# Performance work log

Measured on AMD Instinct MI355X. Metric: run time of the kernel, lower is better.

## Reference

```python
import jax, jax.numpy as jnp
import numpy as np

N_NODES = 100000
N_EDGES = 1000000
NHID = 128
N_CLASSES = 5000


def setup_inputs() -> dict:
    key = jax.random.key(0)
    ks = jax.random.split(key, 8)
    feature = jax.random.normal(ks[0], (N_NODES, NHID), dtype=jnp.float32)
    # Linear weights stored as [in, out] so forward is x @ W + b
    W1 = jax.random.normal(ks[1], (2 * NHID, NHID), dtype=jnp.float32) * (1.0 / np.sqrt(2 * NHID))
    b1 = jnp.zeros((NHID,), dtype=jnp.float32)
    alpha = jnp.full((NHID,), 0.25, dtype=jnp.float32)  # PReLU per-channel init
    W2 = jax.random.normal(ks[2], (NHID, 2), dtype=jnp.float32) * (1.0 / np.sqrt(NHID))
    b2 = jnp.zeros((2,), dtype=jnp.float32)
    row = jax.random.randint(ks[3], (N_EDGES,), 0, N_NODES, dtype=jnp.int64)
    col = jax.random.randint(ks[4], (N_EDGES,), 0, N_NODES, dtype=jnp.int64)
    label = jax.random.randint(ks[5], (N_NODES,), 0, N_CLASSES, dtype=jnp.int64)
    return {"feature": feature, "W1": W1, "b1": b1, "alpha": alpha,
            "W2": W2, "b2": b2, "row": row, "col": col, "label": label}


def reference(feature, W1, b1, alpha, W2, b2, row, col, label):
    # per-edge label: 1 if endpoints share a cluster label
    y = (label[row] == label[col]).astype(jnp.int32)  # [E]
    # edge gather + concat: [E, 2*nhid]
    x = jnp.concatenate([feature[row], feature[col]], axis=1)
    h = x @ W1 + b1                                   # [E, nhid]
    h = jnp.where(h >= 0, h, alpha * h)               # PReLU, per-channel alpha
    logits = h @ W2 + b2                              # [E, 2]
    logp = jax.nn.log_softmax(logits, axis=-1)
    # mean cross-entropy over edges
    loss = -jnp.mean(jnp.take_along_axis(logp, y[:, None], axis=1))
    return loss
```

## Files before the change

kernel.cpp:

```cpp
#include <hip/hip_runtime.h>
#include <hip/hip_bf16.h>

typedef __bf16 bf16_t;
typedef bf16_t bf16x8 __attribute__((ext_vector_type(8)));
typedef float floatx4 __attribute__((ext_vector_type(4)));
typedef float floatx2 __attribute__((ext_vector_type(2)));

#define N_NODES 100000
#define N_EDGES 1000000
#define NHID 128
#define PQ_COLS 256

__global__ __launch_bounds__(256) void k_prep(const float* __restrict__ W1,
                                              const float* __restrict__ b1,
                                              const float* __restrict__ alpha,
                                              const float* __restrict__ W2,
                                              const float* __restrict__ b2,
                                              bf16_t* __restrict__ WT,
                                              float* __restrict__ wabsg,
                                              float* __restrict__ u1g,
                                              float* __restrict__ u2g,
                                              float* __restrict__ constg) {
    __shared__ float w1L[128];
    int i = blockIdx.x * 256 + threadIdx.x;
    if (i < 32768) {
        int n = i >> 7;
        int k = i & 127;
        float v = (n < 128) ? W1[k * 128 + n] : W1[(k + 128) * 128 + (n - 128)];
        WT[i] = (bf16_t)v;
    }
    if (blockIdx.x == 128) {
        int t = threadIdx.x;
        if (t < 128) {
            float wd = W2[2 * t + 1] - W2[2 * t];
            float al = alpha[t];
            w1L[t] = wd * (1.f + al) * 0.5f;
            wabsg[t] = wd * (1.f - al) * 0.5f;
        }
        __syncthreads();
        if (t < 128) {
            float a1 = 0.f, a2 = 0.f;
            for (int j = 0; j < 128; ++j) {
                a1 = fmaf(W1[t * 128 + j], w1L[j], a1);
                a2 = fmaf(W1[(t + 128) * 128 + j], w1L[j], a2);
            }
            u1g[t] = a1;
            u2g[t] = a2;
        }
        if (t == 0) {
            float c = 0.f;
            for (int j = 0; j < 128; ++j) c = fmaf(w1L[j], b1[j], c);
            *constg = c + (b2[1] - b2[0]);
        }
    }
}

__global__ __launch_bounds__(256) void k_gemm_pq(const float* __restrict__ F,
                                                 const bf16_t* __restrict__ WT,
                                                 const float* __restrict__ b1,
                                                 const float* __restrict__ u1g,
                                                 const float* __restrict__ u2g,
                                                 const int* __restrict__ label,
                                                 unsigned char* __restrict__ PQ8,
                                                 float4* __restrict__ aux_g) {
    __shared__ bf16x8 As8[1024];
    __shared__ float sp1[4][64];
    __shared__ float sp2[4][64];
    const int t = threadIdx.x;
    const int m0 = blockIdx.x * 64;

#pragma unroll
    for (int j = 0; j < 8; ++j) {
        int chunk = j * 256 + t;
        int r = chunk >> 5;
        int c4 = chunk & 31;
        int gr = m0 + r;
        float4 u = {0.f, 0.f, 0.f, 0.f};
        if (gr < N_NODES) u = ((const float4*)F)[(size_t)gr * 32 + c4];
        int s    = c4 >> 3;
        int quad = (c4 >> 1) & 3;
        int half = c4 & 1;
        bf16_t* dst = (bf16_t*)&As8[(((r >> 4) * 4 + s) * 4 + quad) * 16 + (r & 15)] + half * 4;
        dst[0] = (bf16_t)u.x; dst[1] = (bf16_t)u.y; dst[2] = (bf16_t)u.z; dst[3] = (bf16_t)u.w;
    }
    __syncthreads();

    const int wave = t >> 6, lane = t & 63;
    const int l15 = lane & 15, quad = lane >> 4;
    const int n0 = wave * 64;

    float bias_v[4];
#pragma unroll
    for (int nt = 0; nt < 4; ++nt) {
        int n = n0 + nt * 16 + l15;
        bias_v[nt] = (n < 128) ? b1[n] : 0.f;
    }

    floatx4 acc[4][4] = {};
#pragma unroll
    for (int s = 0; s < 4; ++s) {
        bf16x8 a[4], b[4];
#pragma unroll
        for (int mt = 0; mt < 4; ++mt)
            a[mt] = As8[(mt * 4 + s) * 64 + lane];
#pragma unroll
        for (int nt = 0; nt < 4; ++nt)
            b[nt] = *(const bf16x8*)(WT + (size_t)(n0 + nt * 16 + l15) * NHID + s * 32 + quad * 8);
#pragma unroll
        for (int mt = 0; mt < 4; ++mt)
#pragma unroll
            for (int nt = 0; nt < 4; ++nt)
                acc[mt][nt] = __builtin_amdgcn_mfma_f32_16x16x32_bf16(a[mt], b[nt], acc[mt][nt], 0, 0, 0);
    }

    {
        int rr = t & 63, part = t >> 6;
        int mt_ = rr >> 4, r15 = rr & 15;
        float a1 = 0.f, a2 = 0.f;
#pragma unroll
        for (int qd = 0; qd < 4; ++qd) {
            bf16x8 av = As8[((mt_ * 4 + part) * 4 + qd) * 16 + r15];
#pragma unroll
            for (int idx = 0; idx < 8; ++idx) {
                float fv = (float)av[idx];
                int kk = part * 32 + qd * 8 + idx;
                a1 = fmaf(fv, u1g[kk], a1);
                a2 = fmaf(fv, u2g[kk], a2);
            }
        }
        sp1[part][rr] = a1;
        sp2[part][rr] = a2;
    }
    __syncthreads();
    if (t < 64) {
        int grow = m0 + t;
        if (grow < N_NODES) {
            float s1 = (sp1[0][t] + sp1[1][t]) + (sp1[2][t] + sp1[3][t]);
            float s2 = (sp2[0][t] + sp2[1][t]) + (sp2[2][t] + sp2[3][t]);
            float4 av = {s1, s2, __int_as_float(label[grow]), 0.f};
            aux_g[grow] = av;
        }
    }

    bf16_t* Tb = (bf16_t*)As8;
#pragma unroll
    for (int h = 0; h < 2; ++h) {
        __syncthreads();
#pragma unroll
        for (int mi = 0; mi < 2; ++mi) {
            int mt = h * 2 + mi;
#pragma unroll
            for (int r = 0; r < 4; ++r) {
                int rl = mi * 16 + quad * 4 + r;
                int sw = ((rl >> 2) & 3) << 4;
#pragma unroll
                for (int nt = 0; nt < 4; ++nt) {
                    int colx = n0 + nt * 16 + l15;
                    Tb[rl * 256 + (colx ^ sw)] = (bf16_t)(acc[mt][nt][r] + bias_v[nt]);
                }
            }
        }
        __syncthreads();
#pragma unroll
        for (int j = 0; j < 4; ++j) {
            int chunk = j * 256 + t;
            int rl  = chunk >> 5;
            int c16 = chunk & 31;
            int grow = m0 + h * 32 + rl;
            if (grow < N_NODES) {
                bf16x8 v = ((bf16x8*)Tb)[rl * 32 + (c16 ^ ((rl >> 2) & 3) * 2)];
                unsigned int lo = 0, hi = 0;
                lo = __builtin_amdgcn_cvt_pk_fp8_f32((float)v[0], (float)v[1], lo, false);
                lo = __builtin_amdgcn_cvt_pk_fp8_f32((float)v[2], (float)v[3], lo, true);
                hi = __builtin_amdgcn_cvt_pk_fp8_f32((float)v[4], (float)v[5], hi, false);
                hi = __builtin_amdgcn_cvt_pk_fp8_f32((float)v[6], (float)v[7], hi, true);
                uint2 pk; pk.x = lo; pk.y = hi;
                ((uint2*)(PQ8 + (size_t)grow * PQ_COLS))[c16] = pk;
            }
        }
    }
}

__global__ __launch_bounds__(256) void k_edge_loss(const unsigned char* __restrict__ PQ8,
                                                   const float4* __restrict__ aux,
                                                   const float* __restrict__ wabsg,
                                                   const float* __restrict__ constg,
                                                   const int* __restrict__ row,
                                                   const int* __restrict__ col,
                                                   float* __restrict__ out) {
    const int lg = threadIdx.x & 15;
    const int group = (blockIdx.x * blockDim.x + threadIdx.x) >> 4;
    const int ng = (gridDim.x * blockDim.x) >> 4;
    const int ch = lg * 8;

    float wabs[8];
#pragma unroll
    for (int j = 0; j < 8; ++j) wabs[j] = wabsg[ch + j];
    const float CB = *constg;

    float acc = 0.f;
    for (int e = group; e < N_EDGES; e += 4 * ng) {
        int ei[4]; bool vl[4];
#pragma unroll
        for (int k = 0; k < 4; ++k) {
            int ee = e + k * ng;
            vl[k] = (ee < N_EDGES);
            ei[k] = vl[k] ? ee : e;
        }
        int r[4], c[4];
#pragma unroll
        for (int k = 0; k < 4; ++k) { r[k] = row[ei[k]]; c[k] = col[ei[k]]; }
        uint2 p[4], q[4];
#pragma unroll
        for (int k = 0; k < 4; ++k) {
            p[k] = *(const uint2*)(PQ8 + (size_t)r[k] * PQ_COLS + ch);
            q[k] = *(const uint2*)(PQ8 + (size_t)c[k] * PQ_COLS + 128 + ch);
        }

        float sab[4] = {0.f, 0.f, 0.f, 0.f};
#pragma unroll
        for (int k = 0; k < 4; ++k) {
            floatx2 p01 = __builtin_amdgcn_cvt_pk_f32_fp8((int)p[k].x, false);
            floatx2 p23 = __builtin_amdgcn_cvt_pk_f32_fp8((int)p[k].x, true);
            floatx2 p45 = __builtin_amdgcn_cvt_pk_f32_fp8((int)p[k].y, false);
            floatx2 p67 = __builtin_amdgcn_cvt_pk_f32_fp8((int)p[k].y, true);
            floatx2 q01 = __builtin_amdgcn_cvt_pk_f32_fp8((int)q[k].x, false);
            floatx2 q23 = __builtin_amdgcn_cvt_pk_f32_fp8((int)q[k].x, true);
            floatx2 q45 = __builtin_amdgcn_cvt_pk_f32_fp8((int)q[k].y, false);
            floatx2 q67 = __builtin_amdgcn_cvt_pk_f32_fp8((int)q[k].y, true);
            floatx2 h01 = p01 + q01;
            floatx2 h23 = p23 + q23;
            floatx2 h45 = p45 + q45;
            floatx2 h67 = p67 + q67;
            float s = sab[k];
            s = fmaf(fabsf(h01[0]), wabs[0], s);
            s = fmaf(fabsf(h01[1]), wabs[1], s);
            s = fmaf(fabsf(h23[0]), wabs[2], s);
            s = fmaf(fabsf(h23[1]), wabs[3], s);
            s = fmaf(fabsf(h45[0]), wabs[4], s);
            s = fmaf(fabsf(h45[1]), wabs[5], s);
            s = fmaf(fabsf(h67[0]), wabs[6], s);
            s = fmaf(fabsf(h67[1]), wabs[7], s);
            sab[k] = s;
        }
#pragma unroll
        for (int m = 8; m >= 1; m >>= 1) {
#pragma unroll
            for (int k = 0; k < 4; ++k) sab[k] += __shfl_xor(sab[k], m, 16);
        }
        if (lg == 0) {
#pragma unroll
            for (int k = 0; k < 4; ++k) {
                float4 ar = aux[r[k]];
                float4 ac2 = aux[c[k]];
                float D = ar.x + ac2.y + CB + sab[k];
                float s = (__float_as_int(ar.z) == __float_as_int(ac2.z)) ? -D : D;
                float loss = fmaxf(s, 0.f) + __logf(1.f + __expf(-fabsf(s)));
                if (vl[k]) acc += loss;
            }
        }
    }
#pragma unroll
    for (int m = 32; m >= 1; m >>= 1) acc += __shfl_xor(acc, m, 64);
    __shared__ float sdata[4];
    int lane = threadIdx.x & 63;
    int wv = threadIdx.x >> 6;
    if (lane == 0) sdata[wv] = acc;
    __syncthreads();
    if (threadIdx.x == 0) {
        float s = (sdata[0] + sdata[1]) + (sdata[2] + sdata[3]);
        atomicAdd(out, s * (1.f / (float)N_EDGES));
    }
}

extern "C" void kernel_launch(void* const* d_in, const int* in_sizes, int n_in,
                              void* d_out, int out_size, void* d_ws, size_t ws_size,
                              hipStream_t stream) {
    const float* feature = (const float*)d_in[0];
    const float* W1      = (const float*)d_in[1];
    const float* b1      = (const float*)d_in[2];
    const float* alpha   = (const float*)d_in[3];
    const float* W2      = (const float*)d_in[4];
    const float* b2      = (const float*)d_in[5];
    const int*   row     = (const int*)d_in[6];
    const int*   col     = (const int*)d_in[7];
    const int*   label   = (const int*)d_in[8];
    float* out = (float*)d_out;

    char* ws = (char*)d_ws;
    unsigned char* PQ8 = (unsigned char*)(ws);
    float4* aux  = (float4*)(ws + 25600000);
    bf16_t* WT   = (bf16_t*)(ws + 27200000);
    float* wabsg = (float*)(ws + 27265536);
    float* u1g   = (float*)(ws + 27266048);
    float* u2g   = (float*)(ws + 27266560);
    float* constg= (float*)(ws + 27267072);

    hipMemsetAsync(d_out, 0, sizeof(float), stream);

    k_prep<<<129, 256, 0, stream>>>(W1, b1, alpha, W2, b2, WT, wabsg, u1g, u2g, constg);
    k_gemm_pq<<<1563, 256, 0, stream>>>(feature, WT, b1, u1g, u2g, label, PQ8, aux);
    k_edge_loss<<<4096, 256, 0, stream>>>(PQ8, aux, wabsg, constg, row, col, out);
}
```

Before: 210.3 us.

## Per-wave 16-row GEMM without LDS staging, permuted PQ layout, wider edge batching

The node GEMM is restructured so each wave handles 16 rows directly from global memory, converting to bf16 in registers and writing fp8 P/Q rows straight from the MFMA accumulators. This removes the LDS staging, transposes and block barriers. The stored channel order becomes permuted, and the abs-weight vector is permuted to match. The edge-loss kernel now processes 8 edges per 16-lane group, spreads the aux gathers and loss math across lanes instead of lane 0, and launches half as many blocks. The cost is higher register pressure and uncoalesced row reads of F in the GEMM.

```diff
diff --git a/kernel.cpp b/kernel.cpp
--- a/kernel.cpp
+++ b/kernel.cpp
@@ -8,8 +8,7 @@
 
 #define N_NODES 100000
 #define N_EDGES 1000000
-#define NHID 128
-#define PQ_COLS 256
+
 
 __global__ __launch_bounds__(256) void k_prep(const float* __restrict__ W1,
                                               const float* __restrict__ b1,
@@ -17,7 +16,7 @@
                                               const float* __restrict__ W2,
                                               const float* __restrict__ b2,
                                               bf16_t* __restrict__ WT,
-                                              float* __restrict__ wabsg,
+                                              float* __restrict__ wabsp,
                                               float* __restrict__ u1g,
                                               float* __restrict__ u2g,
                                               float* __restrict__ constg) {
@@ -35,7 +34,9 @@
             float wd = W2[2 * t + 1] - W2[2 * t];
             float al = alpha[t];
             w1L[t] = wd * (1.f + al) * 0.5f;
-            wabsg[t] = wd * (1.f - al) * 0.5f;
+            int c = (t & 7) * 16 + (t >> 3);
+            float wdc = W2[2 * c + 1] - W2[2 * c];
+            wabsp[t] = wdc * (1.f - alpha[c]) * 0.5f;
         }
         __syncthreads();
         if (t < 128) {
@@ -55,135 +56,91 @@
     }
 }
 
-__global__ __launch_bounds__(256) void k_gemm_pq(const float* __restrict__ F,
-                                                 const bf16_t* __restrict__ WT,
-                                                 const float* __restrict__ b1,
-                                                 const float* __restrict__ u1g,
-                                                 const float* __restrict__ u2g,
-                                                 const int* __restrict__ label,
-                                                 unsigned char* __restrict__ PQ8,
-                                                 float4* __restrict__ aux_g) {
-    __shared__ bf16x8 As8[1024];
-    __shared__ float sp1[4][64];
-    __shared__ float sp2[4][64];
-    const int t = threadIdx.x;
-    const int m0 = blockIdx.x * 64;
-
-#pragma unroll
-    for (int j = 0; j < 8; ++j) {
-        int chunk = j * 256 + t;
-        int r = chunk >> 5;
-        int c4 = chunk & 31;
-        int gr = m0 + r;
-        float4 u = {0.f, 0.f, 0.f, 0.f};
-        if (gr < N_NODES) u = ((const float4*)F)[(size_t)gr * 32 + c4];
-        int s    = c4 >> 3;
-        int quad = (c4 >> 1) & 3;
-        int half = c4 & 1;
-        bf16_t* dst = (bf16_t*)&As8[(((r >> 4) * 4 + s) * 4 + quad) * 16 + (r & 15)] + half * 4;
-        dst[0] = (bf16_t)u.x; dst[1] = (bf16_t)u.y; dst[2] = (bf16_t)u.z; dst[3] = (bf16_t)u.w;
-    }
-    __syncthreads();
-
-    const int wave = t >> 6, lane = t & 63;
+__global__ __launch_bounds__(256) void k_gemm(const float* __restrict__ F,
+                                              const bf16_t* __restrict__ WT,
+                                              const float* __restrict__ b1,
+                                              const float* __restrict__ u1g,
+                                              const float* __restrict__ u2g,
+                                              const int* __restrict__ label,
+                                              unsigned char* __restrict__ PQ8,
+                                              float4* __restrict__ aux_g) {
+    const int lane = threadIdx.x & 63;
+    const int wid = blockIdx.x * 4 + (threadIdx.x >> 6);
+    const int m0 = wid * 16;
+    if (m0 >= N_NODES) return;
     const int l15 = lane & 15, quad = lane >> 4;
-    const int n0 = wave * 64;
-
-    float bias_v[4];
-#pragma unroll
-    for (int nt = 0; nt < 4; ++nt) {
-        int n = n0 + nt * 16 + l15;
-        bias_v[nt] = (n < 128) ? b1[n] : 0.f;
-    }
-
-    floatx4 acc[4][4] = {};
+
+    const float4* Fr = (const float4*)(F + (size_t)(m0 + l15) * 128);
+    floatx4 acc[16] = {};
+    float a1 = 0.f, a2 = 0.f;
+
 #pragma unroll
     for (int s = 0; s < 4; ++s) {
-        bf16x8 a[4], b[4];
-#pragma unroll
-        for (int mt = 0; mt < 4; ++mt)
-            a[mt] = As8[(mt * 4 + s) * 64 + lane];
-#pragma unroll
-        for (int nt = 0; nt < 4; ++nt)
-            b[nt] = *(const bf16x8*)(WT + (size_t)(n0 + nt * 16 + l15) * NHID + s * 32 + quad * 8);
-#pragma unroll
-        for (int mt = 0; mt < 4; ++mt)
-#pragma unroll
-            for (int nt = 0; nt < 4; ++nt)
-                acc[mt][nt] = __builtin_amdgcn_mfma_f32_16x16x32_bf16(a[mt], b[nt], acc[mt][nt], 0, 0, 0);
-    }
-
-    {
-        int rr = t & 63, part = t >> 6;
-        int mt_ = rr >> 4, r15 = rr & 15;
-        float a1 = 0.f, a2 = 0.f;
-#pragma unroll
-        for (int qd = 0; qd < 4; ++qd) {
-            bf16x8 av = As8[((mt_ * 4 + part) * 4 + qd) * 16 + r15];
-#pragma unroll
-            for (int idx = 0; idx < 8; ++idx) {
-                float fv = (float)av[idx];
-                int kk = part * 32 + qd * 8 + idx;
-                a1 = fmaf(fv, u1g[kk], a1);
-                a2 = fmaf(fv, u2g[kk], a2);
-            }
-        }
-        sp1[part][rr] = a1;
-        sp2[part][rr] = a2;
-    }
-    __syncthreads();
-    if (t < 64) {
-        int grow = m0 + t;
-        if (grow < N_NODES) {
-            float s1 = (sp1[0][t] + sp1[1][t]) + (sp1[2][t] + sp1[3][t]);
-            float s2 = (sp2[0][t] + sp2[1][t]) + (sp2[2][t] + sp2[3][t]);
-            float4 av = {s1, s2, __int_as_float(label[grow]), 0.f};
-            aux_g[grow] = av;
-        }
-    }
-
-    bf16_t* Tb = (bf16_t*)As8;
-#pragma unroll
-    for (int h = 0; h < 2; ++h) {
-        __syncthreads();
-#pragma unroll
-        for (int mi = 0; mi < 2; ++mi) {
-            int mt = h * 2 + mi;
-#pragma unroll
-            for (int r = 0; r < 4; ++r) {
-                int rl = mi * 16 + quad * 4 + r;
-                int sw = ((rl >> 2) & 3) << 4;
-#pragma unroll
-                for (int nt = 0; nt < 4; ++nt) {
-                    int colx = n0 + nt * 16 + l15;
-                    Tb[rl * 256 + (colx ^ sw)] = (bf16_t)(acc[mt][nt][r] + bias_v[nt]);
-                }
-            }
-        }
-        __syncthreads();
-#pragma unroll
-        for (int j = 0; j < 4; ++j) {
-            int chunk = j * 256 + t;
-            int rl  = chunk >> 5;
-            int c16 = chunk & 31;
-            int grow = m0 + h * 32 + rl;
-            if (grow < N_NODES) {
-                bf16x8 v = ((bf16x8*)Tb)[rl * 32 + (c16 ^ ((rl >> 2) & 3) * 2)];
-                unsigned int lo = 0, hi = 0;
-                lo = __builtin_amdgcn_cvt_pk_fp8_f32((float)v[0], (float)v[1], lo, false);
-                lo = __builtin_amdgcn_cvt_pk_fp8_f32((float)v[2], (float)v[3], lo, true);
-                hi = __builtin_amdgcn_cvt_pk_fp8_f32((float)v[4], (float)v[5], hi, false);
-                hi = __builtin_amdgcn_cvt_pk_fp8_f32((float)v[6], (float)v[7], hi, true);
-                uint2 pk; pk.x = lo; pk.y = hi;
-                ((uint2*)(PQ8 + (size_t)grow * PQ_COLS))[c16] = pk;
-            }
+        float4 fa = Fr[s * 8 + quad * 2];
+        float4 fb = Fr[s * 8 + quad * 2 + 1];
+        const float* u1p = u1g + s * 32 + quad * 8;
+        const float* u2p = u2g + s * 32 + quad * 8;
+        float fv[8] = {fa.x, fa.y, fa.z, fa.w, fb.x, fb.y, fb.z, fb.w};
+#pragma unroll
+        for (int j = 0; j < 8; ++j) {
+            a1 = fmaf(fv[j], u1p[j], a1);
+            a2 = fmaf(fv[j], u2p[j], a2);
+        }
+        bf16x8 af;
+#pragma unroll
+        for (int j = 0; j < 8; ++j) af[j] = (bf16_t)fv[j];
+
+#pragma unroll
+        for (int g = 0; g < 4; ++g) {
+            bf16x8 bf[4];
+#pragma unroll
+            for (int jj = 0; jj < 4; ++jj)
+                bf[jj] = *(const bf16x8*)(WT + (size_t)((g * 4 + jj) * 16 + l15) * 128 + s * 32 + quad * 8);
+#pragma unroll
+            for (int jj = 0; jj < 4; ++jj)
+                acc[g * 4 + jj] = __builtin_amdgcn_mfma_f32_16x16x32_bf16(af, bf[jj], acc[g * 4 + jj], 0, 0, 0);
+        }
+    }
+
+    a1 += __shfl_xor(a1, 16, 64); a1 += __shfl_xor(a1, 32, 64);
+    a2 += __shfl_xor(a2, 16, 64); a2 += __shfl_xor(a2, 32, 64);
+    if (quad == 0) {
+        int grow = m0 + l15;
+        float4 av = {a1, a2, __int_as_float(label[grow]), 0.f};
+        aux_g[grow] = av;
+    }
+
+    float bv[8];
+#pragma unroll
+    for (int j = 0; j < 8; ++j) bv[j] = b1[j * 16 + l15];
+#pragma unroll
+    for (int r = 0; r < 4; ++r) {
+        int grow = m0 + quad * 4 + r;
+        unsigned char* rowp = PQ8 + (size_t)grow * 256 + l15 * 8;
+        {
+            unsigned int lo = 0, hi = 0;
+            lo = __builtin_amdgcn_cvt_pk_fp8_f32(acc[0][r] + bv[0], acc[1][r] + bv[1], lo, false);
+            lo = __builtin_amdgcn_cvt_pk_fp8_f32(acc[2][r] + bv[2], acc[3][r] + bv[3], lo, true);
+            hi = __builtin_amdgcn_cvt_pk_fp8_f32(acc[4][r] + bv[4], acc[5][r] + bv[5], hi, false);
+            hi = __builtin_amdgcn_cvt_pk_fp8_f32(acc[6][r] + bv[6], acc[7][r] + bv[7], hi, true);
+            uint2 pk; pk.x = lo; pk.y = hi;
+            *(uint2*)(rowp) = pk;
+        }
+        {
+            unsigned int lo = 0, hi = 0;
+            lo = __builtin_amdgcn_cvt_pk_fp8_f32(acc[8][r],  acc[9][r],  lo, false);
+            lo = __builtin_amdgcn_cvt_pk_fp8_f32(acc[10][r], acc[11][r], lo, true);
+            hi = __builtin_amdgcn_cvt_pk_fp8_f32(acc[12][r], acc[13][r], hi, false);
+            hi = __builtin_amdgcn_cvt_pk_fp8_f32(acc[14][r], acc[15][r], hi, true);
+            uint2 pk; pk.x = lo; pk.y = hi;
+            *(uint2*)(rowp + 128) = pk;
         }
     }
 }
 
 __global__ __launch_bounds__(256) void k_edge_loss(const unsigned char* __restrict__ PQ8,
                                                    const float4* __restrict__ aux,
-                                                   const float* __restrict__ wabsg,
+                                                   const float* __restrict__ wabsp,
                                                    const float* __restrict__ constg,
                                                    const int* __restrict__ row,
                                                    const int* __restrict__ col,
@@ -195,31 +152,32 @@
 
     float wabs[8];
 #pragma unroll
-    for (int j = 0; j < 8; ++j) wabs[j] = wabsg[ch + j];
+    for (int j = 0; j < 8; ++j) wabs[j] = wabsp[ch + j];
     const float CB = *constg;
 
     float acc = 0.f;
-    for (int e = group; e < N_EDGES; e += 4 * ng) {
-        int ei[4]; bool vl[4];
-#pragma unroll
-        for (int k = 0; k < 4; ++k) {
+    for (int e = group; e < N_EDGES; e += 8 * ng) {
+        int r[8], c[8];
+#pragma unroll
+        for (int k = 0; k < 8; ++k) {
             int ee = e + k * ng;
-            vl[k] = (ee < N_EDGES);
-            ei[k] = vl[k] ? ee : e;
-        }
-        int r[4], c[4];
-#pragma unroll
-        for (int k = 0; k < 4; ++k) { r[k] = row[ei[k]]; c[k] = col[ei[k]]; }
-        uint2 p[4], q[4];
-#pragma unroll
-        for (int k = 0; k < 4; ++k) {
-            p[k] = *(const uint2*)(PQ8 + (size_t)r[k] * PQ_COLS + ch);
-            q[k] = *(const uint2*)(PQ8 + (size_t)c[k] * PQ_COLS + 128 + ch);
-        }
-
-        float sab[4] = {0.f, 0.f, 0.f, 0.f};
-#pragma unroll
-        for (int k = 0; k < 4; ++k) {
+            int es = (ee < N_EDGES) ? ee : e;
+            r[k] = row[es]; c[k] = col[es];
+        }
+        uint2 p[8], q[8];
+#pragma unroll
+        for (int k = 0; k < 8; ++k) {
+            p[k] = *(const uint2*)(PQ8 + (size_t)r[k] * 256 + ch);
+            q[k] = *(const uint2*)(PQ8 + (size_t)c[k] * 256 + 128 + ch);
+        }
+        int ee2 = e + (lg & 7) * ng;
+        int es2 = (ee2 < N_EDGES) ? ee2 : e;
+        const int* ibase = (lg < 8) ? row : col;
+        float4 a = aux[ibase[es2]];
+
+        float sab[8] = {0.f, 0.f, 0.f, 0.f, 0.f, 0.f, 0.f, 0.f};
+#pragma unroll
+        for (int k = 0; k < 8; ++k) {
             floatx2 p01 = __builtin_amdgcn_cvt_pk_f32_fp8((int)p[k].x, false);
             floatx2 p23 = __builtin_amdgcn_cvt_pk_f32_fp8((int)p[k].x, true);
             floatx2 p45 = __builtin_amdgcn_cvt_pk_f32_fp8((int)p[k].y, false);
@@ -246,19 +204,18 @@
 #pragma unroll
         for (int m = 8; m >= 1; m >>= 1) {
 #pragma unroll
-            for (int k = 0; k < 4; ++k) sab[k] += __shfl_xor(sab[k], m, 16);
-        }
-        if (lg == 0) {
-#pragma unroll
-            for (int k = 0; k < 4; ++k) {
-                float4 ar = aux[r[k]];
-                float4 ac2 = aux[c[k]];
-                float D = ar.x + ac2.y + CB + sab[k];
-                float s = (__float_as_int(ar.z) == __float_as_int(ac2.z)) ? -D : D;
-                float loss = fmaxf(s, 0.f) + __logf(1.f + __expf(-fabsf(s)));
-                if (vl[k]) acc += loss;
-            }
-        }
+            for (int k = 0; k < 8; ++k) sab[k] += __shfl_xor(sab[k], m, 16);
+        }
+        float s2o = __shfl(a.y, (lg + 8) & 15, 16);
+        float lzc = __shfl(a.z, (lg + 8) & 15, 16);
+        float mysab = sab[0];
+#pragma unroll
+        for (int k = 1; k < 8; ++k) mysab = (lg == k) ? sab[k] : mysab;
+        float D = a.x + s2o + CB + mysab;
+        float sgn = (__float_as_int(a.z) == __float_as_int(lzc)) ? -D : D;
+        float loss = fmaxf(sgn, 0.f) + __logf(1.f + __expf(-fabsf(sgn)));
+        bool vld = (lg < 8) && (e + lg * ng < N_EDGES);
+        acc += vld ? loss : 0.f;
     }
 #pragma unroll
     for (int m = 32; m >= 1; m >>= 1) acc += __shfl_xor(acc, m, 64);
@@ -291,14 +248,14 @@
     unsigned char* PQ8 = (unsigned char*)(ws);
     float4* aux  = (float4*)(ws + 25600000);
     bf16_t* WT   = (bf16_t*)(ws + 27200000);
-    float* wabsg = (float*)(ws + 27265536);
+    float* wabsp = (float*)(ws + 27265536);
     float* u1g   = (float*)(ws + 27266048);
     float* u2g   = (float*)(ws + 27266560);
     float* constg= (float*)(ws + 27267072);
 
     hipMemsetAsync(d_out, 0, sizeof(float), stream);
 
-    k_prep<<<129, 256, 0, stream>>>(W1, b1, alpha, W2, b2, WT, wabsg, u1g, u2g, constg);
-    k_gemm_pq<<<1563, 256, 0, stream>>>(feature, WT, b1, u1g, u2g, label, PQ8, aux);
-    k_edge_loss<<<4096, 256, 0, stream>>>(PQ8, aux, wabsg, constg, row, col, out);
-}
+    k_prep<<<129, 256, 0, stream>>>(W1, b1, alpha, W2, b2, WT, wabsp, u1g, u2g, constg);
+    k_gemm<<<1563, 256, 0, stream>>>(feature, WT, b1, u1g, u2g, label, PQ8, aux);
+    k_edge_loss<<<2048, 256, 0, stream>>>(PQ8, aux, wabsp, constg, row, col, out);
+}
```

Result: slower. 218.7 us (+4.0%).
